# Kernel tuning notes

Hardware: AMD Instinct MI355X
Metric: run time of the kernel (lower is better)

The kernel has to match this reference:

```python
import jax, jax.numpy as jnp
import numpy as np

B, T, D, H, S, PM = 2048, 128, 32, 256, 39, 12


def setup_inputs() -> dict:
    key = jax.random.key(0)
    ks = jax.random.split(key, 20)
    s = 0.05
    return {
        "x": jax.random.normal(ks[0], (B, T, D), jnp.float32),
        "latlons": jax.random.normal(ks[1], (B, 2), jnp.float32),
        "yearly_aggs": jax.random.normal(ks[2], (B, 37), jnp.float32),
        "pred_month": jax.random.uniform(ks[3], (B, PM), jnp.float32),
        # EA-LSTM cell parameters (Linear stores weight as [out,in])
        "Wf_i": jax.random.normal(ks[4], (H, D), jnp.float32) * s,
        "Wf_h": jax.random.normal(ks[5], (H, H), jnp.float32) * s,
        "bf_h": jnp.zeros((H,), jnp.float32),
        "Wu": jax.random.normal(ks[6], (H, S), jnp.float32) * s,
        "bu": jnp.zeros((H,), jnp.float32),
        "Wg_i": jax.random.normal(ks[7], (H, D), jnp.float32) * s,
        "Wg_h": jax.random.normal(ks[8], (H, H), jnp.float32) * s,
        "bg_h": jnp.zeros((H,), jnp.float32),
        "Wo_i": jax.random.normal(ks[9], (H, D), jnp.float32) * s,
        "Wo_h": jax.random.normal(ks[10], (H, H), jnp.float32) * s,
        "bo_h": jnp.zeros((H,), jnp.float32),
        # dense head: [268 -> 256 -> 1], no nonlinearity between layers (as in source)
        "Wd0": jax.random.normal(ks[11], (256, H + PM), jnp.float32) * s,
        "bd0": jnp.zeros((256,), jnp.float32),
        "Wd1": jax.random.normal(ks[12], (1, 256), jnp.float32) * s,
        "bd1": jnp.zeros((1,), jnp.float32),
    }


def reference(x, latlons, yearly_aggs, pred_month,
              Wf_i, Wf_h, bf_h, Wu, bu,
              Wg_i, Wg_h, bg_h, Wo_i, Wo_h, bo_h,
              Wd0, bd0, Wd1, bd1):
    x_s = jnp.concatenate([latlons, yearly_aggs], axis=-1)  # [B,S]
    i_gate = jax.nn.sigmoid(x_s @ Wu.T + bu)  # [B,H], static input gate

    # Precompute the input-to-gate projections for all timesteps (one big GEMM each)
    pf = jnp.einsum('btd,hd->tbh', x, Wf_i)  # [T,B,H]
    pg = jnp.einsum('btd,hd->tbh', x, Wg_i)
    po = jnp.einsum('btd,hd->tbh', x, Wo_i)

    h0 = jnp.zeros((x.shape[0], Wf_h.shape[0]), x.dtype)
    c0 = jnp.zeros_like(h0)

    def step(carry, inp):
        h, c = carry
        pf_t, pg_t, po_t = inp
        f = jax.nn.sigmoid(pf_t + h @ Wf_h.T + bf_h)
        g = jnp.tanh(pg_t + h @ Wg_h.T + bg_h)
        o = jax.nn.sigmoid(po_t + h @ Wo_h.T + bo_h)
        c1 = f * c + i_gate * g
        h1 = o * jnp.tanh(c1)
        return (h1, c1), None

    (h_last, _), _ = jax.lax.scan(step, (h0, c0), (pf, pg, po))

    # only the last hidden state feeds the dense head (dropout p=0 -> identity)
    z = jnp.concatenate([h_last, pred_month], axis=-1)  # [B, H+12]
    z = z @ Wd0.T + bd0
    z = z @ Wd1.T + bd1
    return z  # [B,1]
```

## Files before the change

### kernel.cpp

```cpp
#include <hip/hip_runtime.h>

typedef __bf16 bf16x8 __attribute__((ext_vector_type(8)));
typedef float  f32x4  __attribute__((ext_vector_type(4)));
typedef int    v4i    __attribute__((ext_vector_type(4)));

#define LOG2E 1.4426950408889634f

__device__ __forceinline__ float fexp(float x){ return __builtin_amdgcn_exp2f(x * LOG2E); }
__device__ __forceinline__ float sigm(float x){ return __builtin_amdgcn_rcpf(1.0f + fexp(-x)); }
__device__ __forceinline__ float ftanh(float x){
  float r = __builtin_amdgcn_rcpf(1.0f + __builtin_amdgcn_exp2f(-2.0f*LOG2E*x));
  return 2.0f*r - 1.0f;
}
__device__ __forceinline__ f32x4 MFMA(bf16x8 a, bf16x8 b, f32x4 c){
  return __builtin_amdgcn_mfma_f32_16x16x32_bf16(a, b, c, 0, 0, 0);
}
#define BC(w) __builtin_bit_cast(v4i, (w))

#define GRP_A(LEAD, A_, KT_) asm volatile(LEAD                  \
    "v_mfma_f32_16x16x32_bf16 %0, %6, %7, %0\n\t"               \
    "v_mfma_f32_16x16x32_bf16 %1, %6, %8, %1\n\t"               \
    "v_mfma_f32_16x16x32_bf16 %2, %6, %9, %2\n\t"               \
    "v_mfma_f32_16x16x32_bf16 %3, %6, %10, %3\n\t"              \
    "v_mfma_f32_16x16x32_bf16 %4, %6, %11, %4\n\t"              \
    "v_mfma_f32_16x16x32_bf16 %5, %6, %12, %5\n\t"              \
    "s_nop 3"                                                   \
    : "+v"(acc0),"+v"(acc1),"+v"(acc2),"+v"(acc3),"+v"(acc4),"+v"(acc5) \
    : "v"(A_), "a"(awf[(KT_)]),"a"(awf[(KT_)+5]),"a"(awf[(KT_)+10]),    \
      "a"(awf[(KT_)+15]),"a"(awf[(KT_)+20]),"a"(awf[(KT_)+25]))

#define GRP_V(A_, O_) asm volatile(                             \
    "v_mfma_f32_16x16x32_bf16 %0, %6, %7, %0\n\t"               \
    "v_mfma_f32_16x16x32_bf16 %1, %6, %8, %1\n\t"               \
    "v_mfma_f32_16x16x32_bf16 %2, %6, %9, %2\n\t"               \
    "v_mfma_f32_16x16x32_bf16 %3, %6, %10, %3\n\t"              \
    "v_mfma_f32_16x16x32_bf16 %4, %6, %11, %4\n\t"              \
    "v_mfma_f32_16x16x32_bf16 %5, %6, %12, %5\n\t"              \
    "s_nop 3"                                                   \
    : "+v"(acc0),"+v"(acc1),"+v"(acc2),"+v"(acc3),"+v"(acc4),"+v"(acc5) \
    : "v"(A_), "v"(wvf[(O_)]),"v"(wvf[(O_)+2]),"v"(wvf[(O_)+4]),        \
      "v"(wvf[(O_)+6]),"v"(wvf[(O_)+8]),"v"(wvf[(O_)+10]))

#define GRP_LX(A7_, AX_) asm volatile(                          \
    "ds_read_b128 %6, %14\n\t"                                  \
    "ds_read_b128 %7, %14 offset:1024\n\t"                      \
    "ds_read_b128 %8, %14 offset:16384\n\t"                     \
    "ds_read_b128 %9, %14 offset:17408\n\t"                     \
    "ds_read_b128 %10, %14 offset:32768\n\t"                    \
    "ds_read_b128 %11, %14 offset:33792\n\t"                    \
    "s_waitcnt lgkmcnt(0)\n\t"                                  \
    "v_mfma_f32_16x16x32_bf16 %0, %12, %6, %0\n\t"              \
    "v_mfma_f32_16x16x32_bf16 %1, %12, %7, %1\n\t"              \
    "v_mfma_f32_16x16x32_bf16 %2, %12, %8, %2\n\t"              \
    "v_mfma_f32_16x16x32_bf16 %3, %12, %9, %3\n\t"              \
    "v_mfma_f32_16x16x32_bf16 %4, %12, %10, %4\n\t"             \
    "v_mfma_f32_16x16x32_bf16 %5, %12, %11, %5\n\t"             \
    "ds_read_b128 %6, %15\n\t"                                  \
    "ds_read_b128 %7, %15 offset:1024\n\t"                      \
    "ds_read_b128 %8, %15 offset:16384\n\t"                     \
    "ds_read_b128 %9, %15 offset:17408\n\t"                     \
    "ds_read_b128 %10, %15 offset:32768\n\t"                    \
    "ds_read_b128 %11, %15 offset:33792\n\t"                    \
    "s_waitcnt lgkmcnt(0)\n\t"                                  \
    "v_mfma_f32_16x16x32_bf16 %0, %13, %6, %0\n\t"              \
    "v_mfma_f32_16x16x32_bf16 %1, %13, %7, %1\n\t"              \
    "v_mfma_f32_16x16x32_bf16 %2, %13, %8, %2\n\t"              \
    "v_mfma_f32_16x16x32_bf16 %3, %13, %9, %3\n\t"              \
    "v_mfma_f32_16x16x32_bf16 %4, %13, %10, %4\n\t"             \
    "v_mfma_f32_16x16x32_bf16 %5, %13, %11, %5\n\t"             \
    "s_nop 3"                                                   \
    : "+v"(acc0),"+v"(acc1),"+v"(acc2),"+v"(acc3),"+v"(acc4),"+v"(acc5), \
      "=&v"(t0),"=&v"(t1),"=&v"(t2),"=&v"(t3),"=&v"(t4),"=&v"(t5)        \
    : "v"(A7_), "v"(AX_), "v"(waddr0), "v"(waddr1))

#define BARRIER() asm volatile("s_waitcnt lgkmcnt(0)\n\ts_barrier" ::: "memory")

__global__ void
__attribute__((amdgpu_flat_work_group_size(512,512), amdgpu_waves_per_eu(2,2)))
ealstm_kernel(
    const float* __restrict__ x,      const float* __restrict__ latlons,
    const float* __restrict__ yearly, const float* __restrict__ pm,
    const float* __restrict__ Wf_i, const float* __restrict__ Wf_h, const float* __restrict__ bf_h,
    const float* __restrict__ Wu,   const float* __restrict__ bu,
    const float* __restrict__ Wg_i, const float* __restrict__ Wg_h, const float* __restrict__ bg_h,
    const float* __restrict__ Wo_i, const float* __restrict__ Wo_h, const float* __restrict__ bo_h,
    const float* __restrict__ Wd0,  const float* __restrict__ bd0,
    const float* __restrict__ Wd1,  const float* __restrict__ bd1,
    float* __restrict__ out)
{
  __shared__ __align__(16) __bf16 hbuf[2][4096];
  __shared__ __align__(16) __bf16 xbuf[2][16*40];
  __shared__ __align__(16) __bf16 wlds[2*48*512];
  __shared__ __align__(16) float  xs[16*64];

  const int tid  = threadIdx.x;
  const int w    = tid >> 6;
  const int lane = tid & 63;
  const int q    = lane >> 4;
  const int l    = lane & 15;
  const int wgb  = blockIdx.x * 8;

  const float* Wh[3] = {Wf_h, Wg_h, Wo_h};
  const float* Wi[3] = {Wf_i, Wg_i, Wo_i};

  for(int idx = tid; idx < 16*64; idx += 512){
    int m = idx >> 6, k = idx & 63;
    float v = 0.0f;
    if(m < 8){
      int b = wgb + m;
      if(k < 2) v = latlons[b*2 + k];
      else if(k < 39) v = yearly[b*37 + (k-2)];
    }
    xs[idx] = v;
  }
  for(int idx = tid; idx < 2*4096; idx += 512) ((__bf16*)hbuf)[idx] = (__bf16)0.0f;
  {
    int buf = tid >> 8, r = 8 + ((tid >> 5) & 7), c = tid & 31;
    xbuf[buf][r*40 + c] = (__bf16)0.0f;
  }
  if(tid < 256){
    int m = tid >> 5, k = tid & 31;
    xbuf[0][m*40 + k] = (__bf16)x[(size_t)(wgb + m)*4096 + k];
  }
  for(int grp = tid; grp < 2*48*64; grp += 512){
    int frag = grp >> 6, ln = grp & 63;
    int kk = frag / 48, f2 = frag % 48;
    int g = f2 >> 4, nt = f2 & 15;
    int q2 = ln >> 4, l2 = ln & 15;
    int cc = nt*16 + l2;
    const float* p = (kk == 0) ? (Wh[g] + cc*256 + 224 + q2*8)
                               : (Wi[g] + cc*32  + q2*8);
    bf16x8 v;
    #pragma unroll
    for(int j=0;j<8;j++) v[j] = (__bf16)p[j];
    *(bf16x8*)&wlds[frag*512 + ln*8] = v;
  }

  const int  srcl = lane & 31;
  const bool lo   = lane < 32;
  const int  qq4  = (q & 1) * 4;
  const int  colw = w*32 + ((lane & 32) >> 1) + l;
  const int  hwb  = (colw >> 5)*512 + qq4*32 + ((colw >> 3) & 3)*8 + (colw & 7);
  const unsigned waddr0 = (unsigned)(unsigned long long)&wlds[(0*48 + w*2)*512 + lane*8];
  const unsigned waddr1 = waddr0 + 49152u;
  const float b3f = bf_h[colw], b3g = bg_h[colw], b3o = bo_h[colw];

  __syncthreads();

  f32x4 igv;
  {
    float bu0 = bu[w*32 + l], bu1 = bu[w*32 + 16 + l];
    f32x4 iga0 = {bu0,bu0,bu0,bu0};
    f32x4 iga1 = {bu1,bu1,bu1,bu1};
    #pragma unroll
    for(int kt=0; kt<2; kt++){
      bf16x8 a;
      const float* xr = &xs[l*64 + kt*32 + q*8];
      #pragma unroll
      for(int j=0;j<8;j++) a[j] = (__bf16)xr[j];
      #pragma unroll
      for(int n=0;n<2;n++){
        int cc = w*32 + n*16 + l;
        bf16x8 b;
        #pragma unroll
        for(int j=0;j<8;j++){
          int k = kt*32 + q*8 + j;
          b[j] = (__bf16)((k < 39) ? Wu[cc*39 + k] : 0.0f);
        }
        if(n == 0) iga0 = MFMA(a, b, iga0); else iga1 = MFMA(a, b, iga1);
      }
    }
    #pragma unroll
    for(int i=0;i<4;i++){
      float s0 = sigm(iga0[i]);
      float s1 = __shfl(sigm(iga1[i]), srcl);
      igv[i] = lo ? s0 : s1;
    }
  }

  v4i wvf[12];
  #pragma unroll
  for(int f = 0; f < 12; f++){
    int gn = f >> 1, kt = 5 + (f & 1);
    int g = gn >> 1, n = gn & 1;
    int cc = w*32 + n*16 + l;
    const float* p = Wh[g] + cc*256 + kt*32 + q*8;
    f32x4 v0 = *(const f32x4*)p;
    f32x4 v1 = *(const f32x4*)(p + 4);
    bf16x8 v;
    v[0]=(__bf16)v0[0]; v[1]=(__bf16)v0[1]; v[2]=(__bf16)v0[2]; v[3]=(__bf16)v0[3];
    v[4]=(__bf16)v1[0]; v[5]=(__bf16)v1[1]; v[6]=(__bf16)v1[2]; v[7]=(__bf16)v1[3];
    wvf[f] = BC(v);
    if((f & 3) == 3) asm volatile("" ::: "memory");
  }
  v4i awf[30];
  #pragma unroll
  for(int f = 0; f < 30; f++){
    int gn = f / 5, kt = f % 5;
    int g = gn >> 1, n = gn & 1;
    int cc = w*32 + n*16 + l;
    const float* p = Wh[g] + cc*256 + kt*32 + q*8;
    f32x4 v0 = *(const f32x4*)p;
    f32x4 v1 = *(const f32x4*)(p + 4);
    bf16x8 v;
    v[0]=(__bf16)v0[0]; v[1]=(__bf16)v0[1]; v[2]=(__bf16)v0[2]; v[3]=(__bf16)v0[3];
    v[4]=(__bf16)v1[0]; v[5]=(__bf16)v1[1]; v[6]=(__bf16)v1[2]; v[7]=(__bf16)v1[3];
    asm("" : "=a"(awf[f]) : "0"(BC(v)));
    if((f % 5) == 4) asm volatile("" ::: "memory");
  }

  f32x4 cst = {0.f, 0.f, 0.f, 0.f};

  const int xri = (lane >> 2)*40 + (lane & 3)*8;
  const float* xbase = x + (size_t)(wgb + (lane >> 2))*4096 + (lane & 3)*8;
  f32x4 pv0 = {0.f,0.f,0.f,0.f}, pv1 = {0.f,0.f,0.f,0.f};
  if(w == 7 && lane < 32){
    pv0 = *(const f32x4*)(xbase + 32);
    pv1 = *(const f32x4*)(xbase + 36);
  }
  asm volatile("" ::: "memory");

#define LSTM_STEP(T_, CUR_)                                                     \
  {                                                                             \
    if(w == 7 && lane < 32){                                                    \
      if((T_) < 127){                                                           \
        bf16x8 v;                                                               \
        v[0]=(__bf16)pv0[0]; v[1]=(__bf16)pv0[1]; v[2]=(__bf16)pv0[2]; v[3]=(__bf16)pv0[3]; \
        v[4]=(__bf16)pv1[0]; v[5]=(__bf16)pv1[1]; v[6]=(__bf16)pv1[2]; v[7]=(__bf16)pv1[3]; \
        *(bf16x8*)&xbuf[(CUR_) ^ 1][xri] = v;                                   \
      }                                                                         \
      if((T_) < 126){                                                           \
        pv0 = *(const f32x4*)(xbase + ((T_)+2)*32);                             \
        pv1 = *(const f32x4*)(xbase + ((T_)+2)*32 + 4);                         \
      }                                                                         \
    }                                                                           \
    asm volatile("" ::: "memory");                                              \
    f32x4 z4 = {0.f,0.f,0.f,0.f};                                               \
    v4i acc0 = BC(z4), acc1 = BC(z4), acc2 = BC(z4);                            \
    v4i acc3 = BC(z4), acc4 = BC(z4), acc5 = BC(z4);                            \
    v4i t0, t1, t2, t3, t4, t5;                                                 \
    const __bf16* hb = hbuf[CUR_];                                              \
    { v4i a = BC(*(const bf16x8*)&hb[0*512 + l*32 + q*8]); GRP_A("s_nop 3\n\t", a, 0); } \
    { v4i a = BC(*(const bf16x8*)&hb[1*512 + l*32 + q*8]); GRP_A("", a, 1); }   \
    { v4i a = BC(*(const bf16x8*)&hb[2*512 + l*32 + q*8]); GRP_A("", a, 2); }   \
    { v4i a = BC(*(const bf16x8*)&hb[3*512 + l*32 + q*8]); GRP_A("", a, 3); }   \
    { v4i a = BC(*(const bf16x8*)&hb[4*512 + l*32 + q*8]); GRP_A("", a, 4); }   \
    { v4i a = BC(*(const bf16x8*)&hb[5*512 + l*32 + q*8]); GRP_V(a, 0); }       \
    { v4i a = BC(*(const bf16x8*)&hb[6*512 + l*32 + q*8]); GRP_V(a, 1); }       \
    { v4i a7 = BC(*(const bf16x8*)&hb[7*512 + l*32 + q*8]);                     \
      v4i ax = BC(*(const bf16x8*)&xbuf[CUR_][l*40 + q*8]);                     \
      GRP_LX(a7, ax); }                                                         \
    asm volatile("s_nop 7\n\ts_nop 7\n\ts_nop 7"                                \
      : "+v"(acc0),"+v"(acc1),"+v"(acc2),"+v"(acc3),"+v"(acc4),"+v"(acc5));     \
    f32x4 a0 = __builtin_bit_cast(f32x4, acc0);                                 \
    f32x4 a1 = __builtin_bit_cast(f32x4, acc1);                                 \
    f32x4 a2 = __builtin_bit_cast(f32x4, acc2);                                 \
    f32x4 a3 = __builtin_bit_cast(f32x4, acc3);                                 \
    f32x4 a4 = __builtin_bit_cast(f32x4, acc4);                                 \
    f32x4 a5 = __builtin_bit_cast(f32x4, acc5);                                 \
    float f0=a0[0], f1=a0[1], f2=a0[2], f3=a0[3];                               \
    float F0=a1[0], F1=a1[1], F2=a1[2], F3=a1[3];                               \
    float g0=a2[0], g1=a2[1], g2=a2[2], g3=a2[3];                               \
    float G0=a3[0], G1=a3[1], G2=a3[2], G3=a3[3];                               \
    float o0=a4[0], o1=a4[1], o2=a4[2], o3=a4[3];                               \
    float O0=a5[0], O1=a5[1], O2=a5[2], O3=a5[3];                               \
      \
    asm volatile(                                                               \
      "s_nop 3\n\t"                                                             \
      "v_permlane32_swap_b32 %0, %12\n\t"                                       \
      "v_permlane32_swap_b32 %1, %13\n\t"                                       \
      "v_permlane32_swap_b32 %2, %14\n\t"                                       \
      "v_permlane32_swap_b32 %3, %15\n\t"                                       \
      "v_permlane32_swap_b32 %4, %16\n\t"                                       \
      "v_permlane32_swap_b32 %5, %17\n\t"                                       \
      "v_permlane32_swap_b32 %6, %18\n\t"                                       \
      "v_permlane32_swap_b32 %7, %19\n\t"                                       \
      "v_permlane32_swap_b32 %8, %20\n\t"                                       \
      "v_permlane32_swap_b32 %9, %21\n\t"                                       \
      "v_permlane32_swap_b32 %10, %22\n\t"                                      \
      "v_permlane32_swap_b32 %11, %23"                                          \
      : "+v"(f0),"+v"(f1),"+v"(f2),"+v"(f3),                                    \
        "+v"(g0),"+v"(g1),"+v"(g2),"+v"(g3),                                    \
        "+v"(o0),"+v"(o1),"+v"(o2),"+v"(o3),                                    \
        "+v"(F0),"+v"(F1),"+v"(F2),"+v"(F3),                                    \
        "+v"(G0),"+v"(G1),"+v"(G2),"+v"(G3),                                    \
        "+v"(O0),"+v"(O1),"+v"(O2),"+v"(O3));                                   \
    __bf16* hbw = &hbuf[(CUR_) ^ 1][hwb];                                       \
    { float fv=sigm(f0+b3f), gv=ftanh(g0+b3g), ov=sigm(o0+b3o);                 \
      float cc=fv*cst[0]+igv[0]*gv; cst[0]=cc; hbw[0]  = (__bf16)(ov*ftanh(cc)); } \
    { float fv=sigm(f1+b3f), gv=ftanh(g1+b3g), ov=sigm(o1+b3o);                 \
      float cc=fv*cst[1]+igv[1]*gv; cst[1]=cc; hbw[32] = (__bf16)(ov*ftanh(cc)); } \
    { float fv=sigm(f2+b3f), gv=ftanh(g2+b3g), ov=sigm(o2+b3o);                 \
      float cc=fv*cst[2]+igv[2]*gv; cst[2]=cc; hbw[64] = (__bf16)(ov*ftanh(cc)); } \
    { float fv=sigm(f3+b3f), gv=ftanh(g3+b3g), ov=sigm(o3+b3o);                 \
      float cc=fv*cst[3]+igv[3]*gv; cst[3]=cc; hbw[96] = (__bf16)(ov*ftanh(cc)); } \
    BARRIER();                                                                  \
  }

  #pragma unroll 1
  for(int tt = 0; tt < 64; tt++){
    LSTM_STEP(2*tt,     0)
    LSTM_STEP(2*tt + 1, 1)
  }
#undef LSTM_STEP

  f32x4 hd[2];
  { f32x4 z4 = {0.f,0.f,0.f,0.f}; hd[0] = z4; hd[1] = z4; }
  #pragma unroll 2
  for(int kt=0; kt<8; kt++){
    bf16x8 a = *(const bf16x8*)&hbuf[0][kt*512 + l*32 + q*8];
    #pragma unroll
    for(int n=0;n<2;n++){
      int cc = w*32 + n*16 + l;
      const float* p = Wd0 + cc*268 + kt*32 + q*8;
      bf16x8 b;
      #pragma unroll
      for(int j=0;j<8;j++) b[j] = (__bf16)p[j];
      hd[n] = MFMA(a, b, hd[n]);
    }
  }
  {
    bf16x8 a;
    #pragma unroll
    for(int j=0;j<8;j++){
      int k2 = q*8 + j;
      a[j] = (__bf16)((l < 8 && k2 < 12) ? pm[(size_t)(wgb + l)*12 + k2] : 0.0f);
    }
    #pragma unroll
    for(int n=0;n<2;n++){
      int cc = w*32 + n*16 + l;
      bf16x8 b;
      #pragma unroll
      for(int j=0;j<8;j++){
        int k2 = q*8 + j;
        b[j] = (__bf16)((k2 < 12) ? Wd0[cc*268 + 256 + k2] : 0.0f);
      }
      hd[n] = MFMA(a, b, hd[n]);
    }
  }
  float* z1 = (float*)wlds;
  #pragma unroll
  for(int n=0;n<2;n++){
    int cc = w*32 + n*16 + l;
    float bb = bd0[cc];
    #pragma unroll
    for(int i=0;i<4;i++) z1[(q*4 + i)*264 + cc] = hd[n][i] + bb;
  }
  __syncthreads();
  if(tid < 256){
    int row = tid >> 5, seg = tid & 31;
    const float* zr = &z1[row*264 + seg*8];
    const float* wr = Wd1 + seg*8;
    float s = 0.0f;
    #pragma unroll
    for(int j=0;j<8;j++) s += zr[j] * wr[j];
    s += __shfl_xor(s, 1);
    s += __shfl_xor(s, 2);
    s += __shfl_xor(s, 4);
    s += __shfl_xor(s, 8);
    s += __shfl_xor(s, 16);
    if(seg == 0) out[wgb + row] = s + bd1[0];
  }
}

extern "C" void kernel_launch(void* const* d_in, const int* in_sizes, int n_in,
                              void* d_out, int out_size, void* d_ws, size_t ws_size,
                              hipStream_t stream) {
  const float* x       = (const float*)d_in[0];
  const float* latlons = (const float*)d_in[1];
  const float* yearly  = (const float*)d_in[2];
  const float* pm      = (const float*)d_in[3];
  const float* Wf_i    = (const float*)d_in[4];
  const float* Wf_h    = (const float*)d_in[5];
  const float* bf_h    = (const float*)d_in[6];
  const float* Wu      = (const float*)d_in[7];
  const float* bu      = (const float*)d_in[8];
  const float* Wg_i    = (const float*)d_in[9];
  const float* Wg_h    = (const float*)d_in[10];
  const float* bg_h    = (const float*)d_in[11];
  const float* Wo_i    = (const float*)d_in[12];
  const float* Wo_h    = (const float*)d_in[13];
  const float* bo_h    = (const float*)d_in[14];
  const float* Wd0     = (const float*)d_in[15];
  const float* bd0     = (const float*)d_in[16];
  const float* Wd1     = (const float*)d_in[17];
  const float* bd1     = (const float*)d_in[18];

  ealstm_kernel<<<dim3(256), dim3(512), 0, stream>>>(
      x, latlons, yearly, pm,
      Wf_i, Wf_h, bf_h, Wu, bu,
      Wg_i, Wg_h, bg_h, Wo_i, Wo_h, bo_h,
      Wd0, bd0, Wd1, bd1,
      (float*)d_out);
}
```

Measured before the change: 343.8 us.

## Rebalance recurrent weight placement across AGPRs, VGPRs and LDS with padded h layout

Redistributes the recurrent Wh fragments so more stay resident in AGPRs and VGPRs. Only part of Wo_h plus the input weights are now read from LDS, and those reads are interleaved into the MFMA chain in smaller groups. The MFMA accumulators move to AGPRs. The h buffer gets a padded row stride of 40 to reduce LDS bank conflicts, and the x prefetch is spread over all 64 lanes of wave 7. The aim is less LDS traffic and less stall time on the serial per-step critical path, at the cost of higher register pressure and more fragile hand-scheduled asm.

Result: slower. 454.3 us (+32.1%).

```diff
diff --git a/kernel.cpp b/kernel.cpp
--- a/kernel.cpp
+++ b/kernel.cpp
@@ -1,6 +1,7 @@
 #include <hip/hip_runtime.h>
 
 typedef __bf16 bf16x8 __attribute__((ext_vector_type(8)));
+typedef __bf16 bf16x4 __attribute__((ext_vector_type(4)));
 typedef float  f32x4  __attribute__((ext_vector_type(4)));
 typedef int    v4i    __attribute__((ext_vector_type(4)));
 
@@ -17,7 +18,8 @@
 }
 #define BC(w) __builtin_bit_cast(v4i, (w))
 
-#define GRP_A(LEAD, A_, KT_) asm volatile(LEAD                  \
+
+#define GRP_42(LEAD, A_, KT_) asm volatile(LEAD                 \
     "v_mfma_f32_16x16x32_bf16 %0, %6, %7, %0\n\t"               \
     "v_mfma_f32_16x16x32_bf16 %1, %6, %8, %1\n\t"               \
     "v_mfma_f32_16x16x32_bf16 %2, %6, %9, %2\n\t"               \
@@ -25,11 +27,11 @@
     "v_mfma_f32_16x16x32_bf16 %4, %6, %11, %4\n\t"              \
     "v_mfma_f32_16x16x32_bf16 %5, %6, %12, %5\n\t"              \
     "s_nop 3"                                                   \
-    : "+v"(acc0),"+v"(acc1),"+v"(acc2),"+v"(acc3),"+v"(acc4),"+v"(acc5) \
-    : "v"(A_), "a"(awf[(KT_)]),"a"(awf[(KT_)+5]),"a"(awf[(KT_)+10]),    \
-      "a"(awf[(KT_)+15]),"a"(awf[(KT_)+20]),"a"(awf[(KT_)+25]))
-
-#define GRP_V(A_, O_) asm volatile(                             \
+    : "+a"(accf0),"+a"(accf1),"+a"(accg0),"+a"(accg1),"+a"(acco0),"+a"(acco1) \
+    : "v"(A_), "a"(awh[(KT_)]),"a"(awh[8+(KT_)]),"a"(awh[16+(KT_)]),          \
+      "a"(awh[24+(KT_)]),"v"(wvf[6+(KT_)]),"v"(wvf[14+(KT_)]))
+
+#define GRP_33(A_, KT_) asm volatile(                           \
     "v_mfma_f32_16x16x32_bf16 %0, %6, %7, %0\n\t"               \
     "v_mfma_f32_16x16x32_bf16 %1, %6, %8, %1\n\t"               \
     "v_mfma_f32_16x16x32_bf16 %2, %6, %9, %2\n\t"               \
@@ -37,41 +39,68 @@
     "v_mfma_f32_16x16x32_bf16 %4, %6, %11, %4\n\t"              \
     "v_mfma_f32_16x16x32_bf16 %5, %6, %12, %5\n\t"              \
     "s_nop 3"                                                   \
-    : "+v"(acc0),"+v"(acc1),"+v"(acc2),"+v"(acc3),"+v"(acc4),"+v"(acc5) \
-    : "v"(A_), "v"(wvf[(O_)]),"v"(wvf[(O_)+2]),"v"(wvf[(O_)+4]),        \
-      "v"(wvf[(O_)+6]),"v"(wvf[(O_)+8]),"v"(wvf[(O_)+10]))
-
-#define GRP_LX(A7_, AX_) asm volatile(                          \
-    "ds_read_b128 %6, %14\n\t"                                  \
-    "ds_read_b128 %7, %14 offset:1024\n\t"                      \
-    "ds_read_b128 %8, %14 offset:16384\n\t"                     \
-    "ds_read_b128 %9, %14 offset:17408\n\t"                     \
-    "ds_read_b128 %10, %14 offset:32768\n\t"                    \
-    "ds_read_b128 %11, %14 offset:33792\n\t"                    \
+    : "+a"(accf0),"+a"(accf1),"+a"(accg0),"+a"(accg1),"+a"(acco0),"+a"(acco1) \
+    : "v"(A_), "a"(awh[(KT_)]),"a"(awh[8+(KT_)]),"a"(awh[16+(KT_)]),          \
+      "v"(wvf[(KT_)-2]),"v"(wvf[6+(KT_)]),"v"(wvf[14+(KT_)]))
+
+#define GRP_K6(A_) asm volatile(                                \
+    "v_mfma_f32_16x16x32_bf16 %0, %5, %6, %0\n\t"               \
+    "v_mfma_f32_16x16x32_bf16 %1, %5, %7, %1\n\t"               \
+    "v_mfma_f32_16x16x32_bf16 %2, %5, %8, %2\n\t"               \
+    "v_mfma_f32_16x16x32_bf16 %3, %5, %9, %3\n\t"               \
+    "v_mfma_f32_16x16x32_bf16 %4, %5, %10, %4\n\t"              \
+    "s_nop 3"                                                   \
+    : "+a"(accf0),"+a"(accf1),"+a"(accg0),"+a"(accg1),"+a"(acco0) \
+    : "v"(A_), "a"(awh[6]),"a"(awh[14]),"a"(awh[22]),"v"(wvf[4]),"v"(wvf[12]))
+
+#define GRP_K7(A_) asm volatile(                                \
+    "v_mfma_f32_16x16x32_bf16 %0, %5, %6, %0\n\t"               \
+    "v_mfma_f32_16x16x32_bf16 %1, %5, %7, %1\n\t"               \
+    "v_mfma_f32_16x16x32_bf16 %2, %5, %8, %2\n\t"               \
+    "v_mfma_f32_16x16x32_bf16 %3, %5, %9, %3\n\t"               \
+    "v_mfma_f32_16x16x32_bf16 %4, %5, %10, %4\n\t"              \
+    "s_nop 3"                                                   \
+    : "+a"(accf0),"+a"(accf1),"+a"(accg0),"+a"(accg1),"+a"(acco0) \
+    : "v"(A_), "a"(awh[7]),"a"(awh[15]),"a"(awh[23]),"v"(wvf[5]),"v"(wvf[13]))
+
+#define XR1(XAC_) asm volatile(                                 \
+    "ds_read_b128 %0, %5 offset:7168\n\t"                       \
+    "ds_read_b128 %1, %5 offset:6144\n\t"                       \
+    "ds_read_b128 %2, %5\n\t"                                   \
+    "ds_read_b128 %3, %5 offset:1024\n\t"                       \
+    "ds_read_b128 %4, %6"                                       \
+    : "=v"(t0),"=v"(t1),"=v"(t2),"=v"(t3),"=v"(ax)              \
+    : "v"(waddrx), "v"(XAC_))
+
+#define XT0(A6_) asm volatile(                                  \
     "s_waitcnt lgkmcnt(0)\n\t"                                  \
-    "v_mfma_f32_16x16x32_bf16 %0, %12, %6, %0\n\t"              \
-    "v_mfma_f32_16x16x32_bf16 %1, %12, %7, %1\n\t"              \
-    "v_mfma_f32_16x16x32_bf16 %2, %12, %8, %2\n\t"              \
-    "v_mfma_f32_16x16x32_bf16 %3, %12, %9, %3\n\t"              \
-    "v_mfma_f32_16x16x32_bf16 %4, %12, %10, %4\n\t"             \
-    "v_mfma_f32_16x16x32_bf16 %5, %12, %11, %5\n\t"             \
-    "ds_read_b128 %6, %15\n\t"                                  \
-    "ds_read_b128 %7, %15 offset:1024\n\t"                      \
-    "ds_read_b128 %8, %15 offset:16384\n\t"                     \
-    "ds_read_b128 %9, %15 offset:17408\n\t"                     \
-    "ds_read_b128 %10, %15 offset:32768\n\t"                    \
-    "ds_read_b128 %11, %15 offset:33792\n\t"                    \
+    "v_mfma_f32_16x16x32_bf16 %0, %2, %1, %0\n\t"               \
+    "ds_read_b128 %1, %3 offset:2048\n\t"                       \
+    "s_nop 3"                                                   \
+    : "+a"(acco1), "+v"(t0) : "v"(A6_), "v"(waddrx))
+
+#define XT1(A7_, AX_) asm volatile(                             \
     "s_waitcnt lgkmcnt(0)\n\t"                                  \
-    "v_mfma_f32_16x16x32_bf16 %0, %13, %6, %0\n\t"              \
-    "v_mfma_f32_16x16x32_bf16 %1, %13, %7, %1\n\t"              \
-    "v_mfma_f32_16x16x32_bf16 %2, %13, %8, %2\n\t"              \
-    "v_mfma_f32_16x16x32_bf16 %3, %13, %9, %3\n\t"              \
-    "v_mfma_f32_16x16x32_bf16 %4, %13, %10, %4\n\t"             \
-    "v_mfma_f32_16x16x32_bf16 %5, %13, %11, %5\n\t"             \
-    "s_nop 3"                                                   \
-    : "+v"(acc0),"+v"(acc1),"+v"(acc2),"+v"(acc3),"+v"(acc4),"+v"(acc5), \
-      "=&v"(t0),"=&v"(t1),"=&v"(t2),"=&v"(t3),"=&v"(t4),"=&v"(t5)        \
-    : "v"(A7_), "v"(AX_), "v"(waddr0), "v"(waddr1))
+    "v_mfma_f32_16x16x32_bf16 %0, %8, %5, %0\n\t"               \
+    "v_mfma_f32_16x16x32_bf16 %1, %9, %6, %1\n\t"               \
+    "v_mfma_f32_16x16x32_bf16 %2, %9, %7, %2\n\t"               \
+    "v_mfma_f32_16x16x32_bf16 %3, %9, %4, %3\n\t"               \
+    "ds_read_b128 %5, %10 offset:3072\n\t"                      \
+    "ds_read_b128 %6, %10 offset:4096\n\t"                      \
+    "ds_read_b128 %7, %10 offset:5120\n\t"                      \
+    "s_nop 3"                                                   \
+    : "+a"(acco1),"+a"(accf0),"+a"(accf1),"+a"(accg0),          \
+      "+v"(t0),"+v"(t1),"+v"(t2),"+v"(t3)                       \
+    : "v"(A7_),"v"(AX_),"v"(waddrx))
+
+#define XT2(AX_) asm volatile(                                  \
+    "s_waitcnt lgkmcnt(0)\n\t"                                  \
+    "v_mfma_f32_16x16x32_bf16 %0, %3, %4, %0\n\t"               \
+    "v_mfma_f32_16x16x32_bf16 %1, %3, %5, %1\n\t"               \
+    "v_mfma_f32_16x16x32_bf16 %2, %3, %6, %2\n\t"               \
+    "s_nop 3"                                                   \
+    : "+a"(accg1),"+a"(acco0),"+a"(acco1)                       \
+    : "v"(AX_), "v"(t1),"v"(t2),"v"(t3))
 
 #define BARRIER() asm volatile("s_waitcnt lgkmcnt(0)\n\ts_barrier" ::: "memory")
 
@@ -88,10 +117,11 @@
     const float* __restrict__ Wd1,  const float* __restrict__ bd1,
     float* __restrict__ out)
 {
-  __shared__ __align__(16) __bf16 hbuf[2][4096];
-  __shared__ __align__(16) __bf16 xbuf[2][16*40];
-  __shared__ __align__(16) __bf16 wlds[2*48*512];
+  __shared__ __align__(16) __bf16 hbuf[2][5120];
+  __shared__ __align__(16) __bf16 xbuf[2][640];
+  __shared__ __align__(16) __bf16 xw[64*512];
   __shared__ __align__(16) float  xs[16*64];
+  __shared__ __align__(16) float  z1s[8*264];
 
   const int tid  = threadIdx.x;
   const int w    = tid >> 6;
@@ -113,36 +143,39 @@
     }
     xs[idx] = v;
   }
-  for(int idx = tid; idx < 2*4096; idx += 512) ((__bf16*)hbuf)[idx] = (__bf16)0.0f;
-  {
-    int buf = tid >> 8, r = 8 + ((tid >> 5) & 7), c = tid & 31;
-    xbuf[buf][r*40 + c] = (__bf16)0.0f;
-  }
+  for(int idx = tid; idx < 2*5120; idx += 512) ((__bf16*)hbuf)[idx] = (__bf16)0.0f;
+  for(int idx = tid; idx < 2*640; idx += 512) ((__bf16*)xbuf)[idx] = (__bf16)0.0f;
+  __syncthreads();
   if(tid < 256){
     int m = tid >> 5, k = tid & 31;
     xbuf[0][m*40 + k] = (__bf16)x[(size_t)(wgb + m)*4096 + k];
   }
-  for(int grp = tid; grp < 2*48*64; grp += 512){
+  for(int grp = tid; grp < 64*64; grp += 512){
     int frag = grp >> 6, ln = grp & 63;
-    int kk = frag / 48, f2 = frag % 48;
-    int g = f2 >> 4, nt = f2 & 15;
+    int w2 = frag >> 3, j = frag & 7;
     int q2 = ln >> 4, l2 = ln & 15;
-    int cc = nt*16 + l2;
-    const float* p = (kk == 0) ? (Wh[g] + cc*256 + 224 + q2*8)
-                               : (Wi[g] + cc*32  + q2*8);
+    const float* p;
+    if(j < 6){
+      int g = j >> 1, n = j & 1;
+      int cc = w2*32 + n*16 + l2;
+      p = Wi[g] + cc*32 + q2*8;
+    } else {
+      int cc = w2*32 + 16 + l2;
+      p = Wo_h + cc*256 + ((j == 6) ? 224 : 192) + q2*8;
+    }
     bf16x8 v;
     #pragma unroll
-    for(int j=0;j<8;j++) v[j] = (__bf16)p[j];
-    *(bf16x8*)&wlds[frag*512 + ln*8] = v;
+    for(int jj=0;jj<8;jj++) v[jj] = (__bf16)p[jj];
+    *(bf16x8*)&xw[frag*512 + ln*8] = v;
   }
 
   const int  srcl = lane & 31;
   const bool lo   = lane < 32;
   const int  qq4  = (q & 1) * 4;
   const int  colw = w*32 + ((lane & 32) >> 1) + l;
-  const int  hwb  = (colw >> 5)*512 + qq4*32 + ((colw >> 3) & 3)*8 + (colw & 7);
-  const unsigned waddr0 = (unsigned)(unsigned long long)&wlds[(0*48 + w*2)*512 + lane*8];
-  const unsigned waddr1 = waddr0 + 49152u;
+  const int  hwb  = (colw >> 5)*640 + qq4*40 + (colw & 31);
+  const unsigned waddrx = (unsigned)(unsigned long long)&xw[w*4096 + lane*8];
+  const unsigned xA0 = (unsigned)(unsigned long long)&xbuf[0][l*40 + q*8];
   const float b3f = bf_h[colw], b3g = bg_h[colw], b3o = bo_h[colw];
 
   __syncthreads();
@@ -178,10 +211,13 @@
     }
   }
 
-  v4i wvf[12];
+  v4i wvf[20];
   #pragma unroll
-  for(int f = 0; f < 12; f++){
-    int gn = f >> 1, kt = 5 + (f & 1);
+  for(int f = 0; f < 20; f++){
+    int gn, kt;
+    if(f < 6){ gn = 3; kt = 2 + f; }
+    else if(f < 14){ gn = 4; kt = f - 6; }
+    else { gn = 5; kt = f - 14; }
     int g = gn >> 1, n = gn & 1;
     int cc = w*32 + n*16 + l;
     const float* p = Wh[g] + cc*256 + kt*32 + q*8;
@@ -193,10 +229,11 @@
     wvf[f] = BC(v);
     if((f & 3) == 3) asm volatile("" ::: "memory");
   }
-  v4i awf[30];
+  v4i awh[26];
   #pragma unroll
-  for(int f = 0; f < 30; f++){
-    int gn = f / 5, kt = f % 5;
+  for(int f = 0; f < 26; f++){
+    int gn = (f < 24) ? (f >> 3) : 3;
+    int kt = (f < 24) ? (f & 7) : (f - 24);
     int g = gn >> 1, n = gn & 1;
     int cc = w*32 + n*16 + l;
     const float* p = Wh[g] + cc*256 + kt*32 + q*8;
@@ -205,59 +242,59 @@
     bf16x8 v;
     v[0]=(__bf16)v0[0]; v[1]=(__bf16)v0[1]; v[2]=(__bf16)v0[2]; v[3]=(__bf16)v0[3];
     v[4]=(__bf16)v1[0]; v[5]=(__bf16)v1[1]; v[6]=(__bf16)v1[2]; v[7]=(__bf16)v1[3];
-    asm("" : "=a"(awf[f]) : "0"(BC(v)));
-    if((f % 5) == 4) asm volatile("" ::: "memory");
+    asm("" : "=a"(awh[f]) : "0"(BC(v)));
+    if((f & 3) == 3) asm volatile("" ::: "memory");
   }
 
   f32x4 cst = {0.f, 0.f, 0.f, 0.f};
 
-  const int xri = (lane >> 2)*40 + (lane & 3)*8;
-  const float* xbase = x + (size_t)(wgb + (lane >> 2))*4096 + (lane & 3)*8;
-  f32x4 pv0 = {0.f,0.f,0.f,0.f}, pv1 = {0.f,0.f,0.f,0.f};
-  if(w == 7 && lane < 32){
-    pv0 = *(const f32x4*)(xbase + 32);
-    pv1 = *(const f32x4*)(xbase + 36);
-  }
+  const int xri = (lane >> 3)*40 + (lane & 7)*4;
+  const float* xbase = x + (size_t)(wgb + (lane >> 3))*4096 + (lane & 7)*4;
+  f32x4 pv = {0.f,0.f,0.f,0.f};
+  if(w == 7) pv = *(const f32x4*)(xbase + 32);
   asm volatile("" ::: "memory");
 
 #define LSTM_STEP(T_, CUR_)                                                     \
   {                                                                             \
-    if(w == 7 && lane < 32){                                                    \
+    if(w == 7){                                                                 \
       if((T_) < 127){                                                           \
-        bf16x8 v;                                                               \
-        v[0]=(__bf16)pv0[0]; v[1]=(__bf16)pv0[1]; v[2]=(__bf16)pv0[2]; v[3]=(__bf16)pv0[3]; \
-        v[4]=(__bf16)pv1[0]; v[5]=(__bf16)pv1[1]; v[6]=(__bf16)pv1[2]; v[7]=(__bf16)pv1[3]; \
-        *(bf16x8*)&xbuf[(CUR_) ^ 1][xri] = v;                                   \
+        bf16x4 v4;                                                              \
+        v4[0]=(__bf16)pv[0]; v4[1]=(__bf16)pv[1];                               \
+        v4[2]=(__bf16)pv[2]; v4[3]=(__bf16)pv[3];                               \
+        *(bf16x4*)&xbuf[(CUR_) ^ 1][xri] = v4;                                  \
       }                                                                         \
-      if((T_) < 126){                                                           \
-        pv0 = *(const f32x4*)(xbase + ((T_)+2)*32);                             \
-        pv1 = *(const f32x4*)(xbase + ((T_)+2)*32 + 4);                         \
-      }                                                                         \
+      if((T_) < 126) pv = *(const f32x4*)(xbase + ((T_)+2)*32);                 \
     }                                                                           \
     asm volatile("" ::: "memory");                                              \
+    v4i t0, t1, t2, t3, ax;                                                     \
+    { unsigned xAc = xA0 + (CUR_)*1280u; XR1(xAc); }                            \
     f32x4 z4 = {0.f,0.f,0.f,0.f};                                               \
-    v4i acc0 = BC(z4), acc1 = BC(z4), acc2 = BC(z4);                            \
-    v4i acc3 = BC(z4), acc4 = BC(z4), acc5 = BC(z4);                            \
-    v4i t0, t1, t2, t3, t4, t5;                                                 \
+    v4i accf0, accf1, accg0, accg1, acco0, acco1;                               \
+    asm volatile("" : "=a"(accf0) : "0"(BC(z4)));                               \
+    asm volatile("" : "=a"(accf1) : "0"(BC(z4)));                               \
+    asm volatile("" : "=a"(accg0) : "0"(BC(z4)));                               \
+    asm volatile("" : "=a"(accg1) : "0"(BC(z4)));                               \
+    asm volatile("" : "=a"(acco0) : "0"(BC(z4)));                               \
+    asm volatile("" : "=a"(acco1) : "0"(BC(z4)));                               \
     const __bf16* hb = hbuf[CUR_];                                              \
-    { v4i a = BC(*(const bf16x8*)&hb[0*512 + l*32 + q*8]); GRP_A("s_nop 3\n\t", a, 0); } \
-    { v4i a = BC(*(const bf16x8*)&hb[1*512 + l*32 + q*8]); GRP_A("", a, 1); }   \
-    { v4i a = BC(*(const bf16x8*)&hb[2*512 + l*32 + q*8]); GRP_A("", a, 2); }   \
-    { v4i a = BC(*(const bf16x8*)&hb[3*512 + l*32 + q*8]); GRP_A("", a, 3); }   \
-    { v4i a = BC(*(const bf16x8*)&hb[4*512 + l*32 + q*8]); GRP_A("", a, 4); }   \
-    { v4i a = BC(*(const bf16x8*)&hb[5*512 + l*32 + q*8]); GRP_V(a, 0); }       \
-    { v4i a = BC(*(const bf16x8*)&hb[6*512 + l*32 + q*8]); GRP_V(a, 1); }       \
-    { v4i a7 = BC(*(const bf16x8*)&hb[7*512 + l*32 + q*8]);                     \
-      v4i ax = BC(*(const bf16x8*)&xbuf[CUR_][l*40 + q*8]);                     \
-      GRP_LX(a7, ax); }                                                         \
+    { v4i a = BC(*(const bf16x8*)&hb[0*640 + l*40 + q*8]); GRP_42("s_nop 3\n\t", a, 0); } \
+    { v4i a = BC(*(const bf16x8*)&hb[1*640 + l*40 + q*8]); GRP_42("", a, 1); }  \
+    { v4i a = BC(*(const bf16x8*)&hb[2*640 + l*40 + q*8]); GRP_33(a, 2); }      \
+    { v4i a = BC(*(const bf16x8*)&hb[3*640 + l*40 + q*8]); GRP_33(a, 3); }      \
+    { v4i a = BC(*(const bf16x8*)&hb[4*640 + l*40 + q*8]); GRP_33(a, 4); }      \
+    { v4i a = BC(*(const bf16x8*)&hb[5*640 + l*40 + q*8]); GRP_33(a, 5); }      \
+    { v4i a = BC(*(const bf16x8*)&hb[6*640 + l*40 + q*8]); XT0(a); GRP_K6(a); } \
+    { v4i a = BC(*(const bf16x8*)&hb[7*640 + l*40 + q*8]); XT1(a, ax); GRP_K7(a); } \
+    XT2(ax);                                                                    \
+           \
     asm volatile("s_nop 7\n\ts_nop 7\n\ts_nop 7"                                \
-      : "+v"(acc0),"+v"(acc1),"+v"(acc2),"+v"(acc3),"+v"(acc4),"+v"(acc5));     \
-    f32x4 a0 = __builtin_bit_cast(f32x4, acc0);                                 \
-    f32x4 a1 = __builtin_bit_cast(f32x4, acc1);                                 \
-    f32x4 a2 = __builtin_bit_cast(f32x4, acc2);                                 \
-    f32x4 a3 = __builtin_bit_cast(f32x4, acc3);                                 \
-    f32x4 a4 = __builtin_bit_cast(f32x4, acc4);                                 \
-    f32x4 a5 = __builtin_bit_cast(f32x4, acc5);                                 \
+      : "+a"(accf0),"+a"(accf1),"+a"(accg0),"+a"(accg1),"+a"(acco0),"+a"(acco1)); \
+    f32x4 a0 = __builtin_bit_cast(f32x4, accf0);                                \
+    f32x4 a1 = __builtin_bit_cast(f32x4, accf1);                                \
+    f32x4 a2 = __builtin_bit_cast(f32x4, accg0);                                \
+    f32x4 a3 = __builtin_bit_cast(f32x4, accg1);                                \
+    f32x4 a4 = __builtin_bit_cast(f32x4, acco0);                                \
+    f32x4 a5 = __builtin_bit_cast(f32x4, acco1);                                \
     float f0=a0[0], f1=a0[1], f2=a0[2], f3=a0[3];                               \
     float F0=a1[0], F1=a1[1], F2=a1[2], F3=a1[3];                               \
     float g0=a2[0], g1=a2[1], g2=a2[2], g3=a2[3];                               \
@@ -287,13 +324,13 @@
         "+v"(O0),"+v"(O1),"+v"(O2),"+v"(O3));                                   \
     __bf16* hbw = &hbuf[(CUR_) ^ 1][hwb];                                       \
     { float fv=sigm(f0+b3f), gv=ftanh(g0+b3g), ov=sigm(o0+b3o);                 \
-      float cc=fv*cst[0]+igv[0]*gv; cst[0]=cc; hbw[0]  = (__bf16)(ov*ftanh(cc)); } \
+      float cc=fv*cst[0]+igv[0]*gv; cst[0]=cc; hbw[0]   = (__bf16)(ov*ftanh(cc)); } \
     { float fv=sigm(f1+b3f), gv=ftanh(g1+b3g), ov=sigm(o1+b3o);                 \
-      float cc=fv*cst[1]+igv[1]*gv; cst[1]=cc; hbw[32] = (__bf16)(ov*ftanh(cc)); } \
+      float cc=fv*cst[1]+igv[1]*gv; cst[1]=cc; hbw[40]  = (__bf16)(ov*ftanh(cc)); } \
     { float fv=sigm(f2+b3f), gv=ftanh(g2+b3g), ov=sigm(o2+b3o);                 \
-      float cc=fv*cst[2]+igv[2]*gv; cst[2]=cc; hbw[64] = (__bf16)(ov*ftanh(cc)); } \
+      float cc=fv*cst[2]+igv[2]*gv; cst[2]=cc; hbw[80]  = (__bf16)(ov*ftanh(cc)); } \
     { float fv=sigm(f3+b3f), gv=ftanh(g3+b3g), ov=sigm(o3+b3o);                 \
-      float cc=fv*cst[3]+igv[3]*gv; cst[3]=cc; hbw[96] = (__bf16)(ov*ftanh(cc)); } \
+      float cc=fv*cst[3]+igv[3]*gv; cst[3]=cc; hbw[120] = (__bf16)(ov*ftanh(cc)); } \
     BARRIER();                                                                  \
   }
 
@@ -308,7 +345,7 @@
   { f32x4 z4 = {0.f,0.f,0.f,0.f}; hd[0] = z4; hd[1] = z4; }
   #pragma unroll 2
   for(int kt=0; kt<8; kt++){
-    bf16x8 a = *(const bf16x8*)&hbuf[0][kt*512 + l*32 + q*8];
+    bf16x8 a = *(const bf16x8*)&hbuf[0][kt*640 + l*40 + q*8];
     #pragma unroll
     for(int n=0;n<2;n++){
       int cc = w*32 + n*16 + l;
@@ -338,18 +375,19 @@
       hd[n] = MFMA(a, b, hd[n]);
     }
   }
-  float* z1 = (float*)wlds;
-  #pragma unroll
-  for(int n=0;n<2;n++){
-    int cc = w*32 + n*16 + l;
-    float bb = bd0[cc];
-    #pragma unroll
-    for(int i=0;i<4;i++) z1[(q*4 + i)*264 + cc] = hd[n][i] + bb;
+  if(lo){
+    #pragma unroll
+    for(int n=0;n<2;n++){
+      int cc = w*32 + n*16 + l;
+      float bb = bd0[cc];
+      #pragma unroll
+      for(int i=0;i<4;i++) z1s[(q*4 + i)*264 + cc] = hd[n][i] + bb;
+    }
   }
   __syncthreads();
   if(tid < 256){
     int row = tid >> 5, seg = tid & 31;
-    const float* zr = &z1[row*264 + seg*8];
+    const float* zr = &z1s[row*264 + seg*8];
     const float* wr = Wd1 + seg*8;
     float s = 0.0f;
     #pragma unroll
```
